# Performance work log

Hardware: AMD Instinct MI355X
Metric: run time of the kernel (lower is better)

Reference implementation:

```python
import jax, jax.numpy as jnp
import numpy as np
import math

B, T, F, H, A = 32, 2048, 2048, 1024, 512


def setup_inputs() -> dict:
    key = jax.random.key(0)
    ks = jax.random.split(key, 8)
    def xavier(k, shape):
        fan_out, fan_in = shape
        bound = math.sqrt(6.0 / (fan_in + fan_out))
        return jax.random.uniform(k, shape, jnp.float32, -bound, bound)
    return {
        "features": jax.random.normal(ks[0], (B, T, F), jnp.float32),
        "hidden": jax.random.normal(ks[1], (B, H), jnp.float32),
        "W_h": xavier(ks[2], (A, H)),
        "b_h": jnp.zeros((A,), jnp.float32),
        "W_a": xavier(ks[3], (A, F)),
        "b_a": jnp.zeros((A,), jnp.float32),
        "v_w": xavier(ks[4], (1, A)),
        "v_b": jnp.zeros((1,), jnp.float32),
    }


def reference(features, hidden, W_h, b_h, W_a, b_a, v_w, v_b):
    # h_proj: [B, 1, A]; a_proj: [B, T, A]
    h_proj = (hidden @ W_h.T + b_h)[:, None, :]
    a_proj = jnp.einsum('btf,af->bta', features, W_a) + b_a
    # energy: [B, T]
    energy = (jnp.tanh(h_proj + a_proj) @ v_w[0] + v_b[0]) / math.sqrt(W_h.shape[0])
    alpha = jax.nn.softmax(energy, axis=1)
    context = jnp.einsum('bt,btf->bf', alpha, features)
    return (context, alpha)
```

## Files before the change

### kernel.cpp

```cpp
#include <hip/hip_runtime.h>
#include <hip/hip_bf16.h>
#include <math.h>

#define B_ 32
#define T_ 2048
#define F_ 2048
#define H_ 1024
#define A_ 512

typedef __attribute__((ext_vector_type(8))) short short8;
typedef __attribute__((ext_vector_type(4))) float f32x4;

__device__ __forceinline__ unsigned short f2bf(float x) {
  union { float f; unsigned int u; } v; v.f = x;
  unsigned int r = v.u + 0x7FFFu + ((v.u >> 16) & 1u);
  return (unsigned short)(r >> 16);
}

#define GLOAD_LDS16(gp, lp) __builtin_amdgcn_global_load_lds( \
    (const __attribute__((address_space(1))) void*)(gp), \
    (__attribute__((address_space(3))) void*)(lp), 16, 0, 0)

__global__ __launch_bounds__(256) void k_convert_wa(const float* __restrict__ wa,
                                                    unsigned short* __restrict__ out) {
  int i = (blockIdx.x * 256 + threadIdx.x) * 4;
  float4 v = *(const float4*)(wa + i);
  ushort4 o;
  o.x = f2bf(v.x); o.y = f2bf(v.y); o.z = f2bf(v.z); o.w = f2bf(v.w);
  *(ushort4*)(out + i) = o;
}

__global__ __launch_bounds__(256) void k_hproj(const float* __restrict__ hidden,
                                               const float* __restrict__ Wh,
                                               const float* __restrict__ bh,
                                               const float* __restrict__ ba,
                                               float* __restrict__ hcomb) {
  int gw = (blockIdx.x * 256 + threadIdx.x) >> 6;
  int lane = threadIdx.x & 63;
  int b = gw >> 9, a = gw & 511;
  const float* wr = Wh + a * H_;
  const float* hr = hidden + b * H_;
  float acc = 0.f;
  #pragma unroll
  for (int k = 0; k < H_; k += 256) {
    float4 w = *(const float4*)(wr + k + lane * 4);
    float4 h = *(const float4*)(hr + k + lane * 4);
    acc += w.x * h.x + w.y * h.y + w.z * h.z + w.w * h.w;
  }
  #pragma unroll
  for (int off = 32; off; off >>= 1) acc += __shfl_xor(acc, off);
  if (lane == 0) hcomb[gw] = acc + bh[a] + ba[a];
}

__global__ __launch_bounds__(512, 4) void k_energy(
    const float* __restrict__ feat, const unsigned short* __restrict__ wab,
    const float* __restrict__ hcomb, const float* __restrict__ vw,
    const float* __restrict__ vb, float* __restrict__ energy) {
  __shared__ __align__(16) unsigned short Bs[512 * 64];
  __shared__ __align__(16) unsigned short As[64 * 64];
  __shared__ float s_h[512];
  __shared__ float s_v[512];
  __shared__ float e_red[64][4];

  const int tid = threadIdx.x;
  const int lane = tid & 63;
  const int w = tid >> 6;
  const int wm = w >> 2, wn = w & 3;
  const int m0 = blockIdx.x * 64;
  const int bb = m0 >> 11;

  s_h[tid] = hcomb[bb * 512 + tid];
  s_v[tid] = vw[tid];

  f32x4 acc[2][8] = {};

  const int arow = tid >> 3;
  const unsigned short* const awp_base = As + arow * 64 +
      (((((tid & 7) * 16)) ^ ((arow & 7) << 4)) >> 1);
  const float* const aptr = feat + (size_t)(m0 + arow) * F_ + (tid & 7) * 8;

  const int bn = tid >> 3;
  const int blb = (((tid & 7) * 16) ^ ((bn & 7) << 4)) >> 1;
  const unsigned short* const bsrc = wab + bn * 2048 + blb;
  char* const ldsb = (char*)Bs + w * 1024;

  const int lrow = lane & 15;
  const int xbase = ((lane >> 4) * 16) ^ ((lane & 7) << 4);

  for (int ks = 0; ks < 32; ++ks) {
    const int k0 = ks * 64;
    __syncthreads();
    const unsigned short* bs = bsrc + k0;
    #pragma unroll
    for (int r = 0; r < 8; ++r) {
      GLOAD_LDS16(bs + r * (64 * 2048), ldsb + r * 8192);
    }
    float4 av0 = *(const float4*)(aptr + k0);
    float4 av1 = *(const float4*)(aptr + k0 + 4);
    short8 apk;
    apk[0] = (short)f2bf(av0.x); apk[1] = (short)f2bf(av0.y);
    apk[2] = (short)f2bf(av0.z); apk[3] = (short)f2bf(av0.w);
    apk[4] = (short)f2bf(av1.x); apk[5] = (short)f2bf(av1.y);
    apk[6] = (short)f2bf(av1.z); apk[7] = (short)f2bf(av1.w);
    *(short8*)awp_base = apk;
    __syncthreads();
    #pragma unroll
    for (int kk = 0; kk < 2; ++kk) {
      const int xo = (xbase ^ (kk << 6)) >> 1;
      const unsigned short* Ab = As + (wm * 32 + lrow) * 64 + xo;
      short8 a0 = *(const short8*)(Ab);
      short8 a1 = *(const short8*)(Ab + 16 * 64);
      const unsigned short* Bb = Bs + (wn * 128 + lrow) * 64 + xo;
      #pragma unroll
      for (int ni = 0; ni < 8; ++ni) {
        short8 bf = *(const short8*)(Bb + ni * 16 * 64);
        acc[0][ni] = __builtin_amdgcn_mfma_f32_16x16x32_bf16(a0, bf, acc[0][ni], 0, 0, 0);
        acc[1][ni] = __builtin_amdgcn_mfma_f32_16x16x32_bf16(a1, bf, acc[1][ni], 0, 0, 0);
      }
    }
  }

  const float vbv = vb[0];
  #pragma unroll
  for (int mi = 0; mi < 2; ++mi) {
    #pragma unroll
    for (int j = 0; j < 4; ++j) {
      float s = 0.f;
      #pragma unroll
      for (int ni = 0; ni < 8; ++ni) {
        int col = wn * 128 + ni * 16 + lrow;
        float x = acc[mi][ni][j] + s_h[col];
        s += tanhf(x) * s_v[col];
      }
      s += __shfl_xor(s, 1); s += __shfl_xor(s, 2);
      s += __shfl_xor(s, 4); s += __shfl_xor(s, 8);
      if (lrow == 0) e_red[wm * 32 + mi * 16 + (lane >> 4) * 4 + j][wn] = s;
    }
  }
  __syncthreads();
  if (tid < 64) {
    float s = e_red[tid][0] + e_red[tid][1] + e_red[tid][2] + e_red[tid][3];
    energy[m0 + tid] = (s + vbv) * 0.04419417382415922f;
  }
}

__global__ __launch_bounds__(256) void k_softmax(const float* __restrict__ energy,
                                                 float* __restrict__ alpha) {
  const int b = blockIdx.x, tid = threadIdx.x;
  const float* e = energy + b * T_;
  float4 v0 = ((const float4*)e)[tid * 2];
  float4 v1 = ((const float4*)e)[tid * 2 + 1];
  float m = fmaxf(fmaxf(fmaxf(v0.x, v0.y), fmaxf(v0.z, v0.w)),
                  fmaxf(fmaxf(v1.x, v1.y), fmaxf(v1.z, v1.w)));
  #pragma unroll
  for (int off = 32; off; off >>= 1) m = fmaxf(m, __shfl_xor(m, off));
  __shared__ float rmax[4], rsum[4];
  const int lane = tid & 63, wv = tid >> 6;
  if (!lane) rmax[wv] = m;
  __syncthreads();
  m = fmaxf(fmaxf(rmax[0], rmax[1]), fmaxf(rmax[2], rmax[3]));
  float x0 = expf(v0.x - m), x1 = expf(v0.y - m), x2 = expf(v0.z - m), x3 = expf(v0.w - m);
  float x4 = expf(v1.x - m), x5 = expf(v1.y - m), x6 = expf(v1.z - m), x7 = expf(v1.w - m);
  float s = ((x0 + x1) + (x2 + x3)) + ((x4 + x5) + (x6 + x7));
  #pragma unroll
  for (int off = 32; off; off >>= 1) s += __shfl_xor(s, off);
  if (!lane) rsum[wv] = s;
  __syncthreads();
  s = (rsum[0] + rsum[1]) + (rsum[2] + rsum[3]);
  float inv = 1.f / s;
  float4 o0 = {x0 * inv, x1 * inv, x2 * inv, x3 * inv};
  float4 o1 = {x4 * inv, x5 * inv, x6 * inv, x7 * inv};
  float* ao = alpha + b * T_;
  ((float4*)ao)[tid * 2] = o0;
  ((float4*)ao)[tid * 2 + 1] = o1;
}

__global__ __launch_bounds__(256) void k_ctx_partial(const float* __restrict__ feat,
                                                     const float* __restrict__ alpha,
                                                     float* __restrict__ part) {
  const int b = blockIdx.x, fh = blockIdx.y, tc = blockIdx.z;
  const int tid = threadIdx.x;
  __shared__ float sa[256];
  sa[tid] = alpha[b * T_ + tc * 256 + tid];
  __syncthreads();
  const int f = fh * 1024 + tid * 4;
  const float* fp = feat + ((size_t)(b * T_ + tc * 256)) * F_ + f;
  float4 s = {0.f, 0.f, 0.f, 0.f};
  #pragma unroll 4
  for (int t = 0; t < 256; ++t) {
    float a = sa[t];
    float4 v = *(const float4*)(fp + (size_t)t * F_);
    s.x += a * v.x; s.y += a * v.y; s.z += a * v.z; s.w += a * v.w;
  }
  *(float4*)(part + ((size_t)(b * 8 + tc)) * F_ + f) = s;
}

__global__ __launch_bounds__(256) void k_ctx_reduce(const float* __restrict__ part,
                                                    float* __restrict__ ctx) {
  const int i4 = blockIdx.x * 256 + threadIdx.x;
  const int b = i4 >> 9, f4 = i4 & 511;
  const float4* p = (const float4*)part;
  float4 s = {0.f, 0.f, 0.f, 0.f};
  #pragma unroll
  for (int tc = 0; tc < 8; ++tc) {
    float4 v = p[((b * 8 + tc) << 9) + f4];
    s.x += v.x; s.y += v.y; s.z += v.z; s.w += v.w;
  }
  ((float4*)ctx)[i4] = s;
}

extern "C" void kernel_launch(void* const* d_in, const int* in_sizes, int n_in,
                              void* d_out, int out_size, void* d_ws, size_t ws_size,
                              hipStream_t stream) {
  const float* feat   = (const float*)d_in[0];
  const float* hidden = (const float*)d_in[1];
  const float* Wh     = (const float*)d_in[2];
  const float* bh     = (const float*)d_in[3];
  const float* Wa     = (const float*)d_in[4];
  const float* ba     = (const float*)d_in[5];
  const float* vw     = (const float*)d_in[6];
  const float* vb     = (const float*)d_in[7];

  float* ctx   = (float*)d_out;
  float* alpha = (float*)d_out + B_ * T_;

  char* ws = (char*)d_ws;
  unsigned short* wab = (unsigned short*)ws;
  float* hcomb  = (float*)(ws + 2097152);
  float* energy = (float*)(ws + 2097152 + 65536);
  float* part   = (float*)(ws + 2097152 + 65536 + 262144);

  k_convert_wa<<<dim3(1024), dim3(256), 0, stream>>>(Wa, wab);
  k_hproj<<<dim3(4096), dim3(256), 0, stream>>>(hidden, Wh, bh, ba, hcomb);
  k_energy<<<dim3(1024), dim3(512), 0, stream>>>(feat, wab, hcomb, vw, vb, energy);
  k_softmax<<<dim3(32), dim3(256), 0, stream>>>(energy, alpha);
  k_ctx_partial<<<dim3(32, 2, 8), dim3(256), 0, stream>>>(feat, alpha, part);
  k_ctx_reduce<<<dim3(64), dim3(256), 0, stream>>>(part, ctx);
}
```

Baseline: 295.1 us.

## Double-buffer energy GEMM LDS tiles with BK=32 and split context reduction finer

Rewrites the energy GEMM main loop to use double-buffered LDS. The A and B tiles for step t+1 are fetched while MFMAs on step t run, with a single barrier per iteration and a new rotation-based swizzle. The K step shrinks from 64 to 32, and shared memory moves to one manual buffer of about 77KB. Separately, the context partial kernel splits T into 16 chunks instead of 8, giving more blocks at the cost of a larger partial buffer and reduction. Risks include higher LDS use lowering occupancy, and the larger partial buffer possibly overrunning the workspace layout.

```diff
diff --git a/kernel.cpp b/kernel.cpp
--- a/kernel.cpp
+++ b/kernel.cpp
@@ -20,6 +20,11 @@
 #define GLOAD_LDS16(gp, lp) __builtin_amdgcn_global_load_lds( \
     (const __attribute__((address_space(1))) void*)(gp), \
     (__attribute__((address_space(3))) void*)(lp), 16, 0, 0)
+
+#define SBAR   asm volatile("s_barrier" ::: "memory")
+#define WAITV0 asm volatile("s_waitcnt vmcnt(0)" ::: "memory")
+#define WAITL0 asm volatile("s_waitcnt lgkmcnt(0)" ::: "memory")
+#define SCHEDB __builtin_amdgcn_sched_barrier(0)
 
 __global__ __launch_bounds__(256) void k_convert_wa(const float* __restrict__ wa,
                                                     unsigned short* __restrict__ out) {
@@ -43,9 +48,9 @@
   float acc = 0.f;
   #pragma unroll
   for (int k = 0; k < H_; k += 256) {
-    float4 w = *(const float4*)(wr + k + lane * 4);
-    float4 h = *(const float4*)(hr + k + lane * 4);
-    acc += w.x * h.x + w.y * h.y + w.z * h.z + w.w * h.w;
+    float4 wv = *(const float4*)(wr + k + lane * 4);
+    float4 hv = *(const float4*)(hr + k + lane * 4);
+    acc += wv.x * hv.x + wv.y * hv.y + wv.z * hv.z + wv.w * hv.w;
   }
   #pragma unroll
   for (int off = 32; off; off >>= 1) acc += __shfl_xor(acc, off);
@@ -56,70 +61,98 @@
     const float* __restrict__ feat, const unsigned short* __restrict__ wab,
     const float* __restrict__ hcomb, const float* __restrict__ vw,
     const float* __restrict__ vb, float* __restrict__ energy) {
-  __shared__ __align__(16) unsigned short Bs[512 * 64];
-  __shared__ __align__(16) unsigned short As[64 * 64];
-  __shared__ float s_h[512];
-  __shared__ float s_v[512];
-  __shared__ float e_red[64][4];
+  __shared__ __align__(16) char smem[78848];
 
   const int tid = threadIdx.x;
   const int lane = tid & 63;
   const int w = tid >> 6;
   const int wm = w >> 2, wn = w & 3;
+  const int lrow = lane & 15, lk = lane >> 4;
   const int m0 = blockIdx.x * 64;
   const int bb = m0 >> 11;
 
+  float* s_h = (float*)(smem + 73728);
+  float* s_v = (float*)(smem + 75776);
+
+  const unsigned short* bsrc0 = wab + (size_t)(tid >> 2) * 2048 +
+      ((((tid & 3) - ((tid >> 3) & 3)) & 3) << 3);
+  const float* asrc = feat + (size_t)(m0 + (tid >> 3)) * 2048 + ((tid & 7) << 2);
+  const int aw_off = ((tid >> 3) << 6) +
+      ((((((tid >> 1) & 3) + ((tid >> 4) & 3)) & 3)) << 4) + ((tid & 1) << 3);
+
+  const int psl = ((lk + (lrow >> 1)) & 3) << 4;
+  const int a_roff = ((wm * 32 + lrow) << 6) + psl;
+  const int b_roff = ((wn * 128 + lrow) << 6) + psl;
+
+  f32x4 acc[2][8] = {};
+
   s_h[tid] = hcomb[bb * 512 + tid];
   s_v[tid] = vw[tid];
-
-  f32x4 acc[2][8] = {};
-
-  const int arow = tid >> 3;
-  const unsigned short* const awp_base = As + arow * 64 +
-      (((((tid & 7) * 16)) ^ ((arow & 7) << 4)) >> 1);
-  const float* const aptr = feat + (size_t)(m0 + arow) * F_ + (tid & 7) * 8;
-
-  const int bn = tid >> 3;
-  const int blb = (((tid & 7) * 16) ^ ((bn & 7) << 4)) >> 1;
-  const unsigned short* const bsrc = wab + bn * 2048 + blb;
-  char* const ldsb = (char*)Bs + w * 1024;
-
-  const int lrow = lane & 15;
-  const int xbase = ((lane >> 4) * 16) ^ ((lane & 7) << 4);
-
-  for (int ks = 0; ks < 32; ++ks) {
-    const int k0 = ks * 64;
-    __syncthreads();
-    const unsigned short* bs = bsrc + k0;
-    #pragma unroll
-    for (int r = 0; r < 8; ++r) {
-      GLOAD_LDS16(bs + r * (64 * 2048), ldsb + r * 8192);
-    }
-    float4 av0 = *(const float4*)(aptr + k0);
-    float4 av1 = *(const float4*)(aptr + k0 + 4);
-    short8 apk;
-    apk[0] = (short)f2bf(av0.x); apk[1] = (short)f2bf(av0.y);
-    apk[2] = (short)f2bf(av0.z); apk[3] = (short)f2bf(av0.w);
-    apk[4] = (short)f2bf(av1.x); apk[5] = (short)f2bf(av1.y);
-    apk[6] = (short)f2bf(av1.z); apk[7] = (short)f2bf(av1.w);
-    *(short8*)awp_base = apk;
-    __syncthreads();
-    #pragma unroll
-    for (int kk = 0; kk < 2; ++kk) {
-      const int xo = (xbase ^ (kk << 6)) >> 1;
-      const unsigned short* Ab = As + (wm * 32 + lrow) * 64 + xo;
-      short8 a0 = *(const short8*)(Ab);
-      short8 a1 = *(const short8*)(Ab + 16 * 64);
-      const unsigned short* Bb = Bs + (wn * 128 + lrow) * 64 + xo;
-      #pragma unroll
-      for (int ni = 0; ni < 8; ++ni) {
-        short8 bf = *(const short8*)(Bb + ni * 16 * 64);
-        acc[0][ni] = __builtin_amdgcn_mfma_f32_16x16x32_bf16(a0, bf, acc[0][ni], 0, 0, 0);
-        acc[1][ni] = __builtin_amdgcn_mfma_f32_16x16x32_bf16(a1, bf, acc[1][ni], 0, 0, 0);
-      }
-    }
-  }
-
+  {
+    char* bd = smem + (w << 10);
+    GLOAD_LDS16(bsrc0,              bd);
+    GLOAD_LDS16(bsrc0 + 128 * 2048, bd + 8192);
+    GLOAD_LDS16(bsrc0 + 256 * 2048, bd + 16384);
+    GLOAD_LDS16(bsrc0 + 384 * 2048, bd + 24576);
+    float4 av = *(const float4*)(asrc);
+    WAITV0; SCHEDB;
+    ushort4 ap;
+    ap.x = f2bf(av.x); ap.y = f2bf(av.y); ap.z = f2bf(av.z); ap.w = f2bf(av.w);
+    *(ushort4*)(smem + 65536 + aw_off) = ap;
+    WAITL0; SBAR;
+  }
+
+  #pragma unroll 2
+  for (int t = 0; t < 64; ++t) {
+    const int cur = t & 1, nxt = cur ^ 1;
+    const int k1 = ((t + 1) & 63) << 5;
+    const unsigned short* bs = bsrc0 + k1;
+    char* bd = smem + nxt * 32768 + (w << 10);
+    GLOAD_LDS16(bs,              bd);
+    GLOAD_LDS16(bs + 128 * 2048, bd + 8192);
+    GLOAD_LDS16(bs + 256 * 2048, bd + 16384);
+    GLOAD_LDS16(bs + 384 * 2048, bd + 24576);
+    float4 av = *(const float4*)(asrc + k1);
+
+    const char* Ab = smem + 65536 + cur * 4096 + a_roff;
+    const char* Bb = smem + cur * 32768 + b_roff;
+    short8 a0 = *(const short8*)(Ab);
+    short8 a1 = *(const short8*)(Ab + 1024);
+    short8 b0 = *(const short8*)(Bb);
+    short8 b1 = *(const short8*)(Bb + 1024);
+    short8 b2 = *(const short8*)(Bb + 2048);
+    short8 b3 = *(const short8*)(Bb + 3072);
+    acc[0][0] = __builtin_amdgcn_mfma_f32_16x16x32_bf16(a0, b0, acc[0][0], 0, 0, 0);
+    acc[1][0] = __builtin_amdgcn_mfma_f32_16x16x32_bf16(a1, b0, acc[1][0], 0, 0, 0);
+    acc[0][1] = __builtin_amdgcn_mfma_f32_16x16x32_bf16(a0, b1, acc[0][1], 0, 0, 0);
+    acc[1][1] = __builtin_amdgcn_mfma_f32_16x16x32_bf16(a1, b1, acc[1][1], 0, 0, 0);
+    acc[0][2] = __builtin_amdgcn_mfma_f32_16x16x32_bf16(a0, b2, acc[0][2], 0, 0, 0);
+    acc[1][2] = __builtin_amdgcn_mfma_f32_16x16x32_bf16(a1, b2, acc[1][2], 0, 0, 0);
+    acc[0][3] = __builtin_amdgcn_mfma_f32_16x16x32_bf16(a0, b3, acc[0][3], 0, 0, 0);
+    acc[1][3] = __builtin_amdgcn_mfma_f32_16x16x32_bf16(a1, b3, acc[1][3], 0, 0, 0);
+    short8 b4 = *(const short8*)(Bb + 4096);
+    short8 b5 = *(const short8*)(Bb + 5120);
+    short8 b6 = *(const short8*)(Bb + 6144);
+    short8 b7 = *(const short8*)(Bb + 7168);
+    acc[0][4] = __builtin_amdgcn_mfma_f32_16x16x32_bf16(a0, b4, acc[0][4], 0, 0, 0);
+    acc[1][4] = __builtin_amdgcn_mfma_f32_16x16x32_bf16(a1, b4, acc[1][4], 0, 0, 0);
+    acc[0][5] = __builtin_amdgcn_mfma_f32_16x16x32_bf16(a0, b5, acc[0][5], 0, 0, 0);
+    acc[1][5] = __builtin_amdgcn_mfma_f32_16x16x32_bf16(a1, b5, acc[1][5], 0, 0, 0);
+    acc[0][6] = __builtin_amdgcn_mfma_f32_16x16x32_bf16(a0, b6, acc[0][6], 0, 0, 0);
+    acc[1][6] = __builtin_amdgcn_mfma_f32_16x16x32_bf16(a1, b6, acc[1][6], 0, 0, 0);
+    acc[0][7] = __builtin_amdgcn_mfma_f32_16x16x32_bf16(a0, b7, acc[0][7], 0, 0, 0);
+    acc[1][7] = __builtin_amdgcn_mfma_f32_16x16x32_bf16(a1, b7, acc[1][7], 0, 0, 0);
+
+    ushort4 ap;
+    ap.x = f2bf(av.x); ap.y = f2bf(av.y); ap.z = f2bf(av.z); ap.w = f2bf(av.w);
+    *(ushort4*)(smem + 65536 + nxt * 4096 + aw_off) = ap;
+
+    WAITL0;
+    WAITV0;
+    SBAR;
+  }
+
+  float (*e_red)[4] = (float(*)[4])(smem + 77824);
   const float vbv = vb[0];
   #pragma unroll
   for (int mi = 0; mi < 2; ++mi) {
@@ -180,19 +213,19 @@
                                                      float* __restrict__ part) {
   const int b = blockIdx.x, fh = blockIdx.y, tc = blockIdx.z;
   const int tid = threadIdx.x;
-  __shared__ float sa[256];
-  sa[tid] = alpha[b * T_ + tc * 256 + tid];
+  __shared__ float sa[128];
+  if (tid < 128) sa[tid] = alpha[b * T_ + tc * 128 + tid];
   __syncthreads();
   const int f = fh * 1024 + tid * 4;
-  const float* fp = feat + ((size_t)(b * T_ + tc * 256)) * F_ + f;
+  const float* fp = feat + ((size_t)(b * T_ + tc * 128)) * F_ + f;
   float4 s = {0.f, 0.f, 0.f, 0.f};
   #pragma unroll 4
-  for (int t = 0; t < 256; ++t) {
+  for (int t = 0; t < 128; ++t) {
     float a = sa[t];
     float4 v = *(const float4*)(fp + (size_t)t * F_);
     s.x += a * v.x; s.y += a * v.y; s.z += a * v.z; s.w += a * v.w;
   }
-  *(float4*)(part + ((size_t)(b * 8 + tc)) * F_ + f) = s;
+  *(float4*)(part + ((size_t)(b * 16 + tc)) * F_ + f) = s;
 }
 
 __global__ __launch_bounds__(256) void k_ctx_reduce(const float* __restrict__ part,
@@ -202,8 +235,8 @@
   const float4* p = (const float4*)part;
   float4 s = {0.f, 0.f, 0.f, 0.f};
   #pragma unroll
-  for (int tc = 0; tc < 8; ++tc) {
-    float4 v = p[((b * 8 + tc) << 9) + f4];
+  for (int tc = 0; tc < 16; ++tc) {
+    float4 v = p[((b * 16 + tc) << 9) + f4];
     s.x += v.x; s.y += v.y; s.z += v.z; s.w += v.w;
   }
   ((float4*)ctx)[i4] = s;
@@ -234,6 +267,6 @@
   k_hproj<<<dim3(4096), dim3(256), 0, stream>>>(hidden, Wh, bh, ba, hcomb);
   k_energy<<<dim3(1024), dim3(512), 0, stream>>>(feat, wab, hcomb, vw, vb, energy);
   k_softmax<<<dim3(32), dim3(256), 0, stream>>>(energy, alpha);
-  k_ctx_partial<<<dim3(32, 2, 8), dim3(256), 0, stream>>>(feat, alpha, part);
+  k_ctx_partial<<<dim3(32, 2, 16), dim3(256), 0, stream>>>(feat, alpha, part);
   k_ctx_reduce<<<dim3(64), dim3(256), 0, stream>>>(part, ctx);
 }
```

After: 354.6 us. 1.2x slower.

## Write bf16 feature copy in energy kernel and reuse it for context

Applied to the files above, without the earlier changes.

The energy kernel, which already converts feature tiles to bf16 for MFMA, now also stores that bf16 tile to a workspace buffer. The context kernel reads this half-size copy instead of the fp32 features, and its T split changes to 16 chunks of 128. This aims to halve the bytes read in the context pass. In exchange it adds a 256 MB write to the energy kernel, needs a much larger workspace, and reduces context precision to bf16 inputs.

```diff
diff --git a/kernel.cpp b/kernel.cpp
--- a/kernel.cpp
+++ b/kernel.cpp
@@ -15,6 +15,11 @@
   union { float f; unsigned int u; } v; v.f = x;
   unsigned int r = v.u + 0x7FFFu + ((v.u >> 16) & 1u);
   return (unsigned short)(r >> 16);
+}
+
+__device__ __forceinline__ float bf2f(unsigned short u) {
+  union { unsigned int u; float f; } v; v.u = ((unsigned int)u) << 16;
+  return v.f;
 }
 
 #define GLOAD_LDS16(gp, lp) __builtin_amdgcn_global_load_lds( \
@@ -55,7 +60,8 @@
 __global__ __launch_bounds__(512, 4) void k_energy(
     const float* __restrict__ feat, const unsigned short* __restrict__ wab,
     const float* __restrict__ hcomb, const float* __restrict__ vw,
-    const float* __restrict__ vb, float* __restrict__ energy) {
+    const float* __restrict__ vb, float* __restrict__ energy,
+    unsigned short* __restrict__ featb) {
   __shared__ __align__(16) unsigned short Bs[512 * 64];
   __shared__ __align__(16) unsigned short As[64 * 64];
   __shared__ float s_h[512];
@@ -75,9 +81,10 @@
   f32x4 acc[2][8] = {};
 
   const int arow = tid >> 3;
-  const unsigned short* const awp_base = As + arow * 64 +
+  unsigned short* const awp_base = As + arow * 64 +
       (((((tid & 7) * 16)) ^ ((arow & 7) << 4)) >> 1);
   const float* const aptr = feat + (size_t)(m0 + arow) * F_ + (tid & 7) * 8;
+  unsigned short* const fbp = featb + (size_t)(m0 + arow) * F_ + ((tid & 7) << 3);
 
   const int bn = tid >> 3;
   const int blb = (((tid & 7) * 16) ^ ((bn & 7) << 4)) >> 1;
@@ -103,6 +110,7 @@
     apk[4] = (short)f2bf(av1.x); apk[5] = (short)f2bf(av1.y);
     apk[6] = (short)f2bf(av1.z); apk[7] = (short)f2bf(av1.w);
     *(short8*)awp_base = apk;
+    *(short8*)(fbp + k0) = apk;
     __syncthreads();
     #pragma unroll
     for (int kk = 0; kk < 2; ++kk) {
@@ -175,24 +183,36 @@
   ((float4*)ao)[tid * 2 + 1] = o1;
 }
 
-__global__ __launch_bounds__(256) void k_ctx_partial(const float* __restrict__ feat,
+__global__ __launch_bounds__(256) void k_ctx_partial(const unsigned short* __restrict__ featb,
                                                      const float* __restrict__ alpha,
                                                      float* __restrict__ part) {
-  const int b = blockIdx.x, fh = blockIdx.y, tc = blockIdx.z;
+  const int b = blockIdx.x, tc = blockIdx.y;
   const int tid = threadIdx.x;
-  __shared__ float sa[256];
-  sa[tid] = alpha[b * T_ + tc * 256 + tid];
-  __syncthreads();
-  const int f = fh * 1024 + tid * 4;
-  const float* fp = feat + ((size_t)(b * T_ + tc * 256)) * F_ + f;
-  float4 s = {0.f, 0.f, 0.f, 0.f};
+  __shared__ float sa[128];
+  if (tid < 128) sa[tid] = alpha[b * T_ + tc * 128 + tid];
+  __syncthreads();
+  const int col = tid * 8;
+  const unsigned short* fp = featb + ((size_t)(b * T_ + tc * 128)) * F_ + col;
+  float s0 = 0.f, s1 = 0.f, s2 = 0.f, s3 = 0.f;
+  float s4 = 0.f, s5 = 0.f, s6 = 0.f, s7 = 0.f;
   #pragma unroll 4
-  for (int t = 0; t < 256; ++t) {
+  for (int t = 0; t < 128; ++t) {
     float a = sa[t];
-    float4 v = *(const float4*)(fp + (size_t)t * F_);
-    s.x += a * v.x; s.y += a * v.y; s.z += a * v.z; s.w += a * v.w;
-  }
-  *(float4*)(part + ((size_t)(b * 8 + tc)) * F_ + f) = s;
+    short8 v = *(const short8*)(fp + (size_t)t * F_);
+    s0 += a * bf2f((unsigned short)v[0]);
+    s1 += a * bf2f((unsigned short)v[1]);
+    s2 += a * bf2f((unsigned short)v[2]);
+    s3 += a * bf2f((unsigned short)v[3]);
+    s4 += a * bf2f((unsigned short)v[4]);
+    s5 += a * bf2f((unsigned short)v[5]);
+    s6 += a * bf2f((unsigned short)v[6]);
+    s7 += a * bf2f((unsigned short)v[7]);
+  }
+  float* pp = part + ((size_t)(b * 16 + tc)) * F_ + col;
+  float4 o0 = {s0, s1, s2, s3};
+  float4 o1 = {s4, s5, s6, s7};
+  *(float4*)(pp) = o0;
+  *(float4*)(pp + 4) = o1;
 }
 
 __global__ __launch_bounds__(256) void k_ctx_reduce(const float* __restrict__ part,
@@ -202,8 +222,8 @@
   const float4* p = (const float4*)part;
   float4 s = {0.f, 0.f, 0.f, 0.f};
   #pragma unroll
-  for (int tc = 0; tc < 8; ++tc) {
-    float4 v = p[((b * 8 + tc) << 9) + f4];
+  for (int tc = 0; tc < 16; ++tc) {
+    float4 v = p[((b * 16 + tc) << 9) + f4];
     s.x += v.x; s.y += v.y; s.z += v.z; s.w += v.w;
   }
   ((float4*)ctx)[i4] = s;
@@ -228,12 +248,13 @@
   unsigned short* wab = (unsigned short*)ws;
   float* hcomb  = (float*)(ws + 2097152);
   float* energy = (float*)(ws + 2097152 + 65536);
-  float* part   = (float*)(ws + 2097152 + 65536 + 262144);
+  float* part   = (float*)(ws + 4194304);
+  unsigned short* featb = (unsigned short*)(ws + 16777216);
 
   k_convert_wa<<<dim3(1024), dim3(256), 0, stream>>>(Wa, wab);
   k_hproj<<<dim3(4096), dim3(256), 0, stream>>>(hidden, Wh, bh, ba, hcomb);
-  k_energy<<<dim3(1024), dim3(512), 0, stream>>>(feat, wab, hcomb, vw, vb, energy);
+  k_energy<<<dim3(1024), dim3(512), 0, stream>>>(feat, wab, hcomb, vw, vb, energy, featb);
   k_softmax<<<dim3(32), dim3(256), 0, stream>>>(energy, alpha);
-  k_ctx_partial<<<dim3(32, 2, 8), dim3(256), 0, stream>>>(feat, alpha, part);
+  k_ctx_partial<<<dim3(32, 16), dim3(256), 0, stream>>>(featb, alpha, part);
   k_ctx_reduce<<<dim3(64), dim3(256), 0, stream>>>(part, ctx);
 }
```

After: 318.7 us. +8.0%, slower.

## Double energy GEMM M-tile, stagger K order, split context reduction finer

Applied to the files above, without the earlier changes.

The energy kernel now processes 128 rows per block instead of 64. This halves the number of times the bf16 W_a tile is streamed into LDS and doubles MFMA work per B-tile load. Each block starts its K loop at an offset that depends on block parity, to spread concurrent accesses to W_a. The hidden-projection and v values are kept in registers, and the reduction scratch reuses the GEMM LDS buffer. The context partial kernel splits T into 16 chunks instead of 8 for more parallelism, which doubles the partial buffer and reduce work. The larger accumulator set (128 floats per thread) and 80KB of LDS per block raise register pressure and cut occupancy, and may cause spills.

```diff
diff --git a/kernel.cpp b/kernel.cpp
--- a/kernel.cpp
+++ b/kernel.cpp
@@ -56,39 +56,36 @@
     const float* __restrict__ feat, const unsigned short* __restrict__ wab,
     const float* __restrict__ hcomb, const float* __restrict__ vw,
     const float* __restrict__ vb, float* __restrict__ energy) {
-  __shared__ __align__(16) unsigned short Bs[512 * 64];
-  __shared__ __align__(16) unsigned short As[64 * 64];
-  __shared__ float s_h[512];
-  __shared__ float s_v[512];
-  __shared__ float e_red[64][4];
+  __shared__ __align__(16) char smem[81920];
+  unsigned short* const Bs = (unsigned short*)smem;
+  unsigned short* const As = (unsigned short*)(smem + 65536);
 
   const int tid = threadIdx.x;
   const int lane = tid & 63;
   const int w = tid >> 6;
   const int wm = w >> 2, wn = w & 3;
-  const int m0 = blockIdx.x * 64;
+  const int lrow = lane & 15;
+  const int m0 = blockIdx.x * 128;
   const int bb = m0 >> 11;
-
-  s_h[tid] = hcomb[bb * 512 + tid];
-  s_v[tid] = vw[tid];
-
-  f32x4 acc[2][8] = {};
-
-  const int arow = tid >> 3;
-  const unsigned short* const awp_base = As + arow * 64 +
-      (((((tid & 7) * 16)) ^ ((arow & 7) << 4)) >> 1);
-  const float* const aptr = feat + (size_t)(m0 + arow) * F_ + (tid & 7) * 8;
+  const int koff = (blockIdx.x & 1) << 4;
+
+  f32x4 acc[4][8] = {};
+
+  const int arow = tid >> 2;
+  const float* const aptr = feat + (size_t)(m0 + arow) * F_ + ((tid & 3) << 4);
+  const int s0 = (tid & 3) << 1;
+  unsigned short* const awp0 = As + arow * 64 + (((s0)     ^ (arow & 7)) << 3);
+  unsigned short* const awp1 = As + arow * 64 + (((s0 + 1) ^ (arow & 7)) << 3);
 
   const int bn = tid >> 3;
   const int blb = (((tid & 7) * 16) ^ ((bn & 7) << 4)) >> 1;
   const unsigned short* const bsrc = wab + bn * 2048 + blb;
   char* const ldsb = (char*)Bs + w * 1024;
 
-  const int lrow = lane & 15;
   const int xbase = ((lane >> 4) * 16) ^ ((lane & 7) << 4);
 
-  for (int ks = 0; ks < 32; ++ks) {
-    const int k0 = ks * 64;
+  for (int t = 0; t < 32; ++t) {
+    const int k0 = ((t + koff) & 31) << 6;
     __syncthreads();
     const unsigned short* bs = bsrc + k0;
     #pragma unroll
@@ -97,48 +94,67 @@
     }
     float4 av0 = *(const float4*)(aptr + k0);
     float4 av1 = *(const float4*)(aptr + k0 + 4);
-    short8 apk;
-    apk[0] = (short)f2bf(av0.x); apk[1] = (short)f2bf(av0.y);
-    apk[2] = (short)f2bf(av0.z); apk[3] = (short)f2bf(av0.w);
-    apk[4] = (short)f2bf(av1.x); apk[5] = (short)f2bf(av1.y);
-    apk[6] = (short)f2bf(av1.z); apk[7] = (short)f2bf(av1.w);
-    *(short8*)awp_base = apk;
+    float4 av2 = *(const float4*)(aptr + k0 + 8);
+    float4 av3 = *(const float4*)(aptr + k0 + 12);
+    short8 p0, p1;
+    p0[0] = (short)f2bf(av0.x); p0[1] = (short)f2bf(av0.y);
+    p0[2] = (short)f2bf(av0.z); p0[3] = (short)f2bf(av0.w);
+    p0[4] = (short)f2bf(av1.x); p0[5] = (short)f2bf(av1.y);
+    p0[6] = (short)f2bf(av1.z); p0[7] = (short)f2bf(av1.w);
+    p1[0] = (short)f2bf(av2.x); p1[1] = (short)f2bf(av2.y);
+    p1[2] = (short)f2bf(av2.z); p1[3] = (short)f2bf(av2.w);
+    p1[4] = (short)f2bf(av3.x); p1[5] = (short)f2bf(av3.y);
+    p1[6] = (short)f2bf(av3.z); p1[7] = (short)f2bf(av3.w);
+    *(short8*)awp0 = p0;
+    *(short8*)awp1 = p1;
     __syncthreads();
     #pragma unroll
     for (int kk = 0; kk < 2; ++kk) {
       const int xo = (xbase ^ (kk << 6)) >> 1;
-      const unsigned short* Ab = As + (wm * 32 + lrow) * 64 + xo;
+      const unsigned short* Ab = As + (wm * 64 + lrow) * 64 + xo;
       short8 a0 = *(const short8*)(Ab);
       short8 a1 = *(const short8*)(Ab + 16 * 64);
+      short8 a2 = *(const short8*)(Ab + 32 * 64);
+      short8 a3 = *(const short8*)(Ab + 48 * 64);
       const unsigned short* Bb = Bs + (wn * 128 + lrow) * 64 + xo;
       #pragma unroll
       for (int ni = 0; ni < 8; ++ni) {
         short8 bf = *(const short8*)(Bb + ni * 16 * 64);
         acc[0][ni] = __builtin_amdgcn_mfma_f32_16x16x32_bf16(a0, bf, acc[0][ni], 0, 0, 0);
         acc[1][ni] = __builtin_amdgcn_mfma_f32_16x16x32_bf16(a1, bf, acc[1][ni], 0, 0, 0);
+        acc[2][ni] = __builtin_amdgcn_mfma_f32_16x16x32_bf16(a2, bf, acc[2][ni], 0, 0, 0);
+        acc[3][ni] = __builtin_amdgcn_mfma_f32_16x16x32_bf16(a3, bf, acc[3][ni], 0, 0, 0);
       }
     }
   }
 
+  float hv[8], vv[8];
+  #pragma unroll
+  for (int ni = 0; ni < 8; ++ni) {
+    int col = wn * 128 + ni * 16 + lrow;
+    hv[ni] = hcomb[bb * 512 + col];
+    vv[ni] = vw[col];
+  }
   const float vbv = vb[0];
-  #pragma unroll
-  for (int mi = 0; mi < 2; ++mi) {
+  float (*e_red)[4] = (float(*)[4])smem;
+  __syncthreads();
+  #pragma unroll
+  for (int mi = 0; mi < 4; ++mi) {
     #pragma unroll
     for (int j = 0; j < 4; ++j) {
       float s = 0.f;
       #pragma unroll
       for (int ni = 0; ni < 8; ++ni) {
-        int col = wn * 128 + ni * 16 + lrow;
-        float x = acc[mi][ni][j] + s_h[col];
-        s += tanhf(x) * s_v[col];
+        float x = acc[mi][ni][j] + hv[ni];
+        s += tanhf(x) * vv[ni];
       }
       s += __shfl_xor(s, 1); s += __shfl_xor(s, 2);
       s += __shfl_xor(s, 4); s += __shfl_xor(s, 8);
-      if (lrow == 0) e_red[wm * 32 + mi * 16 + (lane >> 4) * 4 + j][wn] = s;
+      if (lrow == 0) e_red[wm * 64 + mi * 16 + (lane >> 4) * 4 + j][wn] = s;
     }
   }
   __syncthreads();
-  if (tid < 64) {
+  if (tid < 128) {
     float s = e_red[tid][0] + e_red[tid][1] + e_red[tid][2] + e_red[tid][3];
     energy[m0 + tid] = (s + vbv) * 0.04419417382415922f;
   }
@@ -180,19 +196,19 @@
                                                      float* __restrict__ part) {
   const int b = blockIdx.x, fh = blockIdx.y, tc = blockIdx.z;
   const int tid = threadIdx.x;
-  __shared__ float sa[256];
-  sa[tid] = alpha[b * T_ + tc * 256 + tid];
+  __shared__ float sa[128];
+  if (tid < 128) sa[tid] = alpha[b * T_ + tc * 128 + tid];
   __syncthreads();
   const int f = fh * 1024 + tid * 4;
-  const float* fp = feat + ((size_t)(b * T_ + tc * 256)) * F_ + f;
+  const float* fp = feat + ((size_t)(b * T_ + tc * 128)) * F_ + f;
   float4 s = {0.f, 0.f, 0.f, 0.f};
   #pragma unroll 4
-  for (int t = 0; t < 256; ++t) {
+  for (int t = 0; t < 128; ++t) {
     float a = sa[t];
     float4 v = *(const float4*)(fp + (size_t)t * F_);
     s.x += a * v.x; s.y += a * v.y; s.z += a * v.z; s.w += a * v.w;
   }
-  *(float4*)(part + ((size_t)(b * 8 + tc)) * F_ + f) = s;
+  *(float4*)(part + ((size_t)(b * 16 + tc)) * F_ + f) = s;
 }
 
 __global__ __launch_bounds__(256) void k_ctx_reduce(const float* __restrict__ part,
@@ -202,8 +218,8 @@
   const float4* p = (const float4*)part;
   float4 s = {0.f, 0.f, 0.f, 0.f};
   #pragma unroll
-  for (int tc = 0; tc < 8; ++tc) {
-    float4 v = p[((b * 8 + tc) << 9) + f4];
+  for (int tc = 0; tc < 16; ++tc) {
+    float4 v = p[((b * 16 + tc) << 9) + f4];
     s.x += v.x; s.y += v.y; s.z += v.z; s.w += v.w;
   }
   ((float4*)ctx)[i4] = s;
@@ -232,8 +248,8 @@
 
   k_convert_wa<<<dim3(1024), dim3(256), 0, stream>>>(Wa, wab);
   k_hproj<<<dim3(4096), dim3(256), 0, stream>>>(hidden, Wh, bh, ba, hcomb);
-  k_energy<<<dim3(1024), dim3(512), 0, stream>>>(feat, wab, hcomb, vw, vb, energy);
+  k_energy<<<dim3(512), dim3(512), 0, stream>>>(feat, wab, hcomb, vw, vb, energy);
   k_softmax<<<dim3(32), dim3(256), 0, stream>>>(energy, alpha);
-  k_ctx_partial<<<dim3(32, 2, 8), dim3(256), 0, stream>>>(feat, alpha, part);
+  k_ctx_partial<<<dim3(32, 2, 16), dim3(256), 0, stream>>>(feat, alpha, part);
   k_ctx_reduce<<<dim3(64), dim3(256), 0, stream>>>(part, ctx);
 }
```

Result: slower. 888.4 us (+201.0%).
